# Performance work log

Hardware: AMD Instinct MI355X
Metric: run time of the kernel (lower is better)

Reference implementation:

```python
import jax, jax.numpy as jnp
import numpy as np

N_HEADS = 16


def setup_inputs() -> dict:
    key = jax.random.key(0)
    ks = jax.random.split(key, 10)
    B, M, N, C, D = 2, 2048, 2048, 1024, 1024
    s = 0.02
    return {
        "kv": jax.random.normal(ks[0], (B, M, C), jnp.float32),
        "q": jax.random.normal(ks[1], (B, N, D), jnp.float32),
        "Wk": jax.random.normal(ks[2], (C, D), jnp.float32) * s,
        "bk": jnp.zeros((D,), jnp.float32),
        "Wq": jax.random.normal(ks[3], (D, D), jnp.float32) * s,
        "bq": jnp.zeros((D,), jnp.float32),
        "Wv": jax.random.normal(ks[4], (C, D), jnp.float32) * s,
        "bv": jnp.zeros((D,), jnp.float32),
        "Wp": jax.random.normal(ks[5], (D, D), jnp.float32) * s,
        "bp": jnp.zeros((D,), jnp.float32),
    }


def reference(kv, q, Wk, bk, Wq, bq, Wv, bv, Wp, bp):
    B, M, C = kv.shape
    B2, N, D = q.shape
    H = N_HEADS
    hd = D // H
    # projections (weights stored as [in, out]; torch Linear is x @ W.T + b with W [out,in])
    k = (kv @ Wk + bk).reshape(B, M, H, hd).transpose(0, 2, 1, 3)  # [B,H,M,hd]
    qh = (q @ Wq + bq).reshape(B, N, H, hd).transpose(0, 2, 1, 3)  # [B,H,N,hd]
    v = (kv @ Wv + bv).reshape(B, M, H, hd).transpose(0, 2, 1, 3)  # [B,H,M,hd]
    scale = 1.0 / jnp.sqrt(jnp.asarray(hd, k.dtype))
    att = jnp.einsum("bhnd,bhmd->bhnm", qh, k) * scale
    att = jax.nn.softmax(att, axis=-1)
    y = jnp.einsum("bhnm,bhmd->bhnd", att, v)  # [B,H,N,hd]
    y = y.transpose(0, 2, 1, 3).reshape(B, N, D)
    return y @ Wp + bp
```

## Files before the change

kernel.cpp:

```cpp
#include <hip/hip_runtime.h>

#define DV 1024
#define HD 64

typedef short v4s __attribute__((ext_vector_type(4)));
typedef short v8s __attribute__((ext_vector_type(8)));
typedef float v4f __attribute__((ext_vector_type(4)));

__device__ __forceinline__ short f2bf(float x){
  unsigned u = __float_as_uint(x);
  u += 0x7FFFu + ((u >> 16) & 1u);
  return (short)(u >> 16);
}

__device__ __forceinline__ void async16(const void* g, void* l){
  __builtin_amdgcn_global_load_lds((const __attribute__((address_space(1))) void*)g,
                                   (__attribute__((address_space(3))) void*)l, 16, 0, 0);
}

__device__ __forceinline__ int swz(int lane){
  return (((lane & 7) ^ (lane >> 3)) << 3);
}

__global__ __launch_bounds__(256) void cvt2(const float* __restrict__ xa,
                                            const float* __restrict__ xb,
                                            short* __restrict__ ya,
                                            short* __restrict__ yb, int n){
  const float* x = blockIdx.y ? xb : xa;
  short* y = blockIdx.y ? yb : ya;
  int stride = gridDim.x * 256 * 4;
  for (int i = (blockIdx.x * 256 + threadIdx.x) * 4; i < n; i += stride){
    float4 v = *(const float4*)(x + i);
    v4s s; s.x = f2bf(v.x); s.y = f2bf(v.y); s.z = f2bf(v.z); s.w = f2bf(v.w);
    *(v4s*)(y + i) = s;
  }
}

__global__ __launch_bounds__(256) void tcvt4(
    const float* __restrict__ W0, const float* __restrict__ W1,
    const float* __restrict__ W2, const float* __restrict__ W3,
    short* __restrict__ T0, short* __restrict__ T1,
    short* __restrict__ T2, short* __restrict__ T3){
  const float* W; short* Wt;
  switch (blockIdx.z){
    case 0: W = W0; Wt = T0; break;
    case 1: W = W1; Wt = T1; break;
    case 2: W = W2; Wt = T2; break;
    default: W = W3; Wt = T3; break;
  }
  __shared__ short L[64 * 68];
  const int t = threadIdx.x;
  const int k0 = blockIdx.y * 64, n0 = blockIdx.x * 64;
  const int rr = t >> 4, cc = (t & 15) * 4;
  #pragma unroll
  for (int j = 0; j < 4; j++){
    int r = rr + j * 16;
    float4 v = *(const float4*)(W + (size_t)(k0 + r) * DV + n0 + cc);
    v4s s; s.x = f2bf(v.x); s.y = f2bf(v.y); s.z = f2bf(v.z); s.w = f2bf(v.w);
    *(v4s*)&L[r * 68 + cc] = s;
  }
  __syncthreads();
  #pragma unroll
  for (int j = 0; j < 4; j++){
    int n = rr + j * 16;
    v4s s;
    s.x = L[(cc + 0) * 68 + n];
    s.y = L[(cc + 1) * 68 + n];
    s.z = L[(cc + 2) * 68 + n];
    s.w = L[(cc + 3) * 68 + n];
    *(v4s*)(Wt + (size_t)(n0 + n) * DV + k0 + cc) = s;
  }
}

template<typename OUT_T>
__device__ __forceinline__ void gemm_tile(
    const short* __restrict__ A, const short* __restrict__ Bt,
    const float* __restrict__ bias, OUT_T* __restrict__ C,
    int M, int N, int K, float out_scale, int m0, int n0, bool bias_row)
{
  __shared__ short As[128 * 64];
  __shared__ short Bs[128 * 64];
  const int tid = threadIdx.x;
  const int wave = tid >> 6, lane = tid & 63;
  const int quad = lane >> 4, l15 = lane & 15;
  const int wr = (wave >> 1) * 64, wc = (wave & 1) * 64;
  const int srow = lane >> 3;
  const int sw = swz(lane);
  const v4f vzero = {0.f, 0.f, 0.f, 0.f};

  const short* pa[4]; const short* pb[4];
  #pragma unroll
  for (int ii = 0; ii < 4; ii++){
    int i = wave * 4 + ii;
    pa[ii] = A  + (size_t)(m0 + i * 8 + srow) * K + sw;
    pb[ii] = Bt + (size_t)(n0 + i * 8 + srow) * K + sw;
  }

  v8s ra[4], rb[4];
  #pragma unroll
  for (int ii = 0; ii < 4; ii++){
    ra[ii] = *(const v8s*)(pa[ii]);
    rb[ii] = *(const v8s*)(pb[ii]);
  }

  v4f acc[4][4];
  #pragma unroll
  for (int i = 0; i < 4; i++)
    #pragma unroll
    for (int j = 0; j < 4; j++)
      acc[i][j] = vzero;

  for (int kt = 0; kt < K; kt += 64){
    __syncthreads();
    #pragma unroll
    for (int ii = 0; ii < 4; ii++){
      int i = wave * 4 + ii;
      *(v8s*)&As[i * 512 + lane * 8] = ra[ii];
      *(v8s*)&Bs[i * 512 + lane * 8] = rb[ii];
    }
    __syncthreads();
    if (kt + 64 < K){
      #pragma unroll
      for (int ii = 0; ii < 4; ii++){
        ra[ii] = *(const v8s*)(pa[ii] + kt + 64);
        rb[ii] = *(const v8s*)(pb[ii] + kt + 64);
      }
    }
    #pragma unroll
    for (int ks = 0; ks < 2; ks++){
      v8s a[4], b[4];
      #pragma unroll
      for (int mt = 0; mt < 4; mt++)
        a[mt] = *(const v8s*)&As[(wr + mt * 16 + l15) * 64 + (((ks * 4 + quad) ^ (l15 & 7)) << 3)];
      #pragma unroll
      for (int nt = 0; nt < 4; nt++)
        b[nt] = *(const v8s*)&Bs[(wc + nt * 16 + l15) * 64 + (((ks * 4 + quad) ^ (l15 & 7)) << 3)];
      #pragma unroll
      for (int mt = 0; mt < 4; mt++)
        #pragma unroll
        for (int nt = 0; nt < 4; nt++)
          acc[mt][nt] = __builtin_amdgcn_mfma_f32_16x16x32_bf16(a[mt], b[nt], acc[mt][nt], 0, 0, 0);
    }
  }

  #pragma unroll
  for (int mt = 0; mt < 4; mt++){
    #pragma unroll
    for (int nt = 0; nt < 4; nt++){
      int row = m0 + wr + mt * 16 + quad * 4;
      int col = n0 + wc + nt * 16 + l15;
      float bcol = bias_row ? 0.0f : bias[col];
      #pragma unroll
      for (int r = 0; r < 4; r++){
        float bv = bias_row ? bias[row + r] : bcol;
        float v = (acc[mt][nt][r] + bv) * out_scale;
        if (sizeof(OUT_T) == 2)
          ((short*)C)[(size_t)(row + r) * N + col] = f2bf(v);
        else
          ((float*)C)[(size_t)(row + r) * N + col] = v;
      }
    }
  }
}

__global__ __launch_bounds__(256, 3) void proj3(
    const short* __restrict__ qb, const short* __restrict__ kvb,
    const short* __restrict__ Wqt, const short* __restrict__ Wkt,
    const short* __restrict__ Wvt,
    const float* __restrict__ bq, const float* __restrict__ bk,
    const float* __restrict__ bv,
    short* __restrict__ Qp, short* __restrict__ Kp, short* __restrict__ VT,
    float qscale)
{
  int bid = blockIdx.x;
  const short *A, *Bt; const float* bias; short* C;
  int M, N, m0, n0; float scale; bool brow;
  if (bid < 512){
    int z = bid >> 8, l = bid & 255;
    M = 4096; N = 1024; m0 = (l & 31) * 128; n0 = (l >> 5) * 128;
    A = z ? kvb : qb; Bt = z ? Wkt : Wqt; bias = z ? bk : bq;
    C = z ? Kp : Qp; scale = z ? 1.0f : qscale; brow = false;
  } else {
    int l = bid - 512;
    M = 1024; N = 4096; m0 = (l >> 5) * 128; n0 = (l & 31) * 128;
    A = Wvt; Bt = kvb; bias = bv; C = VT; scale = 1.0f; brow = true;
  }
  gemm_tile<short>(A, Bt, bias, C, M, N, 1024, scale, m0, n0, brow);
}

__global__ __launch_bounds__(256, 3) void gemm_f32(
    const short* __restrict__ A, const short* __restrict__ Bt,
    const float* __restrict__ bias, float* __restrict__ C)
{
  int bid = blockIdx.x;
  gemm_tile<float>(A, Bt, bias, C, 4096, 1024, 1024, 1.0f,
                   (bid & 31) * 128, (bid >> 5) * 128, false);
}

__global__ __launch_bounds__(256, 4) void attn(
    const short* __restrict__ Qp, const short* __restrict__ Kp,
    const short* __restrict__ Vt, short* __restrict__ Y)
{
  __shared__ short Qs[64 * 64];
  __shared__ short Ks[64 * 64];
  __shared__ short Vs[64 * 64];
  const int tid = threadIdx.x;
  const int wave = tid >> 6, lane = tid & 63;
  const int quad = lane >> 4, l15 = lane & 15;
  const int gid = blockIdx.x;
  const int qi = gid >> 5, bh = gid & 31;
  const int h = bh & 15, b = bh >> 4;
  const int n0 = qi * 64;
  const int srow = lane >> 3;
  const int sw = swz(lane);
  const size_t rowbase = (size_t)b * 2048;
  const v4f vzero = {0.f, 0.f, 0.f, 0.f};

  #pragma unroll
  for (int ii = 0; ii < 2; ii++){
    int i = wave * 2 + ii;
    async16(Qp + (rowbase + n0 + i * 8 + srow) * DV + h * HD + sw, &Qs[i * 512]);
  }

  const short* pk[2]; const short* pv[2];
  #pragma unroll
  for (int ii = 0; ii < 2; ii++){
    int i = wave * 2 + ii;
    pk[ii] = Kp + (rowbase + i * 8 + srow) * DV + h * HD + sw;
    pv[ii] = Vt + (size_t)(h * HD + i * 8 + srow) * 4096 + rowbase + sw;
  }
  v8s rk[2], rv[2];
  #pragma unroll
  for (int ii = 0; ii < 2; ii++){ rk[ii] = *(const v8s*)(pk[ii]); rv[ii] = *(const v8s*)(pv[ii]); }

  __syncthreads();

  v8s qf[2];
  #pragma unroll
  for (int ks = 0; ks < 2; ks++)
    qf[ks] = *(const v8s*)&Qs[(wave * 16 + l15) * 64 + (((ks * 4 + quad) ^ (l15 & 7)) << 3)];

  v4f o[4];
  #pragma unroll
  for (int dt = 0; dt < 4; dt++) o[dt] = vzero;
  float lsum = 0.0f;

  for (int kt = 0; kt < 32; kt++){
    __syncthreads();
    #pragma unroll
    for (int ii = 0; ii < 2; ii++){
      int i = wave * 2 + ii;
      *(v8s*)&Ks[i * 512 + lane * 8] = rk[ii];
      *(v8s*)&Vs[i * 512 + lane * 8] = rv[ii];
    }
    __syncthreads();
    if (kt < 31){
      #pragma unroll
      for (int ii = 0; ii < 2; ii++){
        rk[ii] = *(const v8s*)(pk[ii] + (size_t)(kt + 1) * 64 * DV);
        rv[ii] = *(const v8s*)(pv[ii] + (kt + 1) * 64);
      }
    }

    v4f s[4];
    #pragma unroll
    for (int kvt = 0; kvt < 4; kvt++) s[kvt] = vzero;
    #pragma unroll
    for (int ks = 0; ks < 2; ks++){
      v8s a[4];
      #pragma unroll
      for (int kvt = 0; kvt < 4; kvt++)
        a[kvt] = *(const v8s*)&Ks[(kvt * 16 + l15) * 64 + (((ks * 4 + quad) ^ (l15 & 7)) << 3)];
      #pragma unroll
      for (int kvt = 0; kvt < 4; kvt++)
        s[kvt] = __builtin_amdgcn_mfma_f32_16x16x32_bf16(a[kvt], qf[ks], s[kvt], 0, 0, 0);
    }

    v4s pf[4];
    #pragma unroll
    for (int kvt = 0; kvt < 4; kvt++){
      float p0 = __builtin_amdgcn_exp2f(s[kvt][0]);
      float p1 = __builtin_amdgcn_exp2f(s[kvt][1]);
      float p2 = __builtin_amdgcn_exp2f(s[kvt][2]);
      float p3 = __builtin_amdgcn_exp2f(s[kvt][3]);
      lsum += (p0 + p1) + (p2 + p3);
      v4s pk4; pk4.x = f2bf(p0); pk4.y = f2bf(p1); pk4.z = f2bf(p2); pk4.w = f2bf(p3);
      pf[kvt] = pk4;
    }

    #pragma unroll
    for (int ks = 0; ks < 4; ks++){
      v4s a[4];
      #pragma unroll
      for (int dt = 0; dt < 4; dt++){
        int vc = ks * 16 + quad * 4;
        a[dt] = *(const v4s*)&Vs[(dt * 16 + l15) * 64 + (((vc >> 3) ^ (l15 & 7)) << 3) + (vc & 7)];
      }
      #pragma unroll
      for (int dt = 0; dt < 4; dt++)
        o[dt] = __builtin_amdgcn_mfma_f32_16x16x16bf16_1k(a[dt], pf[ks], o[dt], 0, 0, 0);
    }
  }

  lsum += __shfl_xor(lsum, 16);
  lsum += __shfl_xor(lsum, 32);
  float inv = 1.0f / lsum;
  size_t row = rowbase + n0 + wave * 16 + l15;
  #pragma unroll
  for (int dt = 0; dt < 4; dt++){
    int col = h * HD + dt * 16 + quad * 4;
    unsigned p0 = (unsigned short)f2bf(o[dt][0] * inv) |
                  ((unsigned)(unsigned short)f2bf(o[dt][1] * inv) << 16);
    unsigned p1 = (unsigned short)f2bf(o[dt][2] * inv) |
                  ((unsigned)(unsigned short)f2bf(o[dt][3] * inv) << 16);
    *(unsigned*)(Y + row * DV + col)     = p0;
    *(unsigned*)(Y + row * DV + col + 2) = p1;
  }
}

extern "C" void kernel_launch(void* const* d_in, const int* in_sizes, int n_in,
                              void* d_out, int out_size, void* d_ws, size_t ws_size,
                              hipStream_t stream) {
  const float* kv = (const float*)d_in[0];
  const float* q  = (const float*)d_in[1];
  const float* Wk = (const float*)d_in[2];
  const float* bk = (const float*)d_in[3];
  const float* Wq = (const float*)d_in[4];
  const float* bq = (const float*)d_in[5];
  const float* Wv = (const float*)d_in[6];
  const float* bv = (const float*)d_in[7];
  const float* Wp = (const float*)d_in[8];
  const float* bp = (const float*)d_in[9];

  const size_t E  = 4194304;
  const size_t WE = 1048576;
  short* p   = (short*)d_ws;
  short* kvb = p; p += E;
  short* qb  = p; p += E;
  short* Wkt = p; p += WE;
  short* Wqt = p; p += WE;
  short* Wvt = p; p += WE;
  short* Wpt = p; p += WE;
  short* Kp  = p; p += E;
  short* Qp  = p; p += E;
  short* VT  = p; p += E;
  short* Yb  = p; p += E;

  cvt2<<<dim3(512, 2), 256, 0, stream>>>(kv, q, kvb, qb, (int)E);
  tcvt4<<<dim3(16, 16, 4), 256, 0, stream>>>(Wk, Wq, Wv, Wp, Wkt, Wqt, Wvt, Wpt);

  proj3<<<768, 256, 0, stream>>>(qb, kvb, Wqt, Wkt, Wvt, bq, bk, bv,
                                 Qp, Kp, VT, 0.18033688011f);

  attn<<<1024, 256, 0, stream>>>(Qp, Kp, VT, Yb);

  gemm_f32<<<256, 256, 0, stream>>>(Yb, Wpt, bp, (float*)d_out);
}
```

Before: 216.8 us.

## Rework attention tiling, bf16 packing and output GEMM tile shape

The attention kernel now processes two KV tiles per barrier pair with double-buffered register prefetch. It loads Q fragments directly from global memory instead of through LDS and stores V in padded rows rather than XOR swizzle. It also packs bf16 with a cheaper round-half-up and byte-permute, which slightly changes rounding. The output projection gets a dedicated 128x64-tile GEMM with twice as many blocks for better occupancy. These changes aim to reduce barrier count, instruction overhead and tail underutilization, at the cost of more registers and LDS.

```diff
diff --git a/kernel.cpp b/kernel.cpp
--- a/kernel.cpp
+++ b/kernel.cpp
@@ -6,16 +6,12 @@
 typedef short v4s __attribute__((ext_vector_type(4)));
 typedef short v8s __attribute__((ext_vector_type(8)));
 typedef float v4f __attribute__((ext_vector_type(4)));
+typedef int   v2i __attribute__((ext_vector_type(2)));
 
 __device__ __forceinline__ short f2bf(float x){
   unsigned u = __float_as_uint(x);
   u += 0x7FFFu + ((u >> 16) & 1u);
   return (short)(u >> 16);
-}
-
-__device__ __forceinline__ void async16(const void* g, void* l){
-  __builtin_amdgcn_global_load_lds((const __attribute__((address_space(1))) void*)g,
-                                   (__attribute__((address_space(3))) void*)l, 16, 0, 0);
 }
 
 __device__ __forceinline__ int swz(int lane){
@@ -188,22 +184,93 @@
   gemm_tile<short>(A, Bt, bias, C, M, N, 1024, scale, m0, n0, brow);
 }
 
-__global__ __launch_bounds__(256, 3) void gemm_f32(
+__global__ __launch_bounds__(256, 2) void gemm_f32(
     const short* __restrict__ A, const short* __restrict__ Bt,
     const float* __restrict__ bias, float* __restrict__ C)
 {
-  int bid = blockIdx.x;
-  gemm_tile<float>(A, Bt, bias, C, 4096, 1024, 1024, 1.0f,
-                   (bid & 31) * 128, (bid >> 5) * 128, false);
+  __shared__ short As[128 * 64];
+  __shared__ short Bs[64 * 64];
+  const int tid = threadIdx.x;
+  const int wave = tid >> 6, lane = tid & 63;
+  const int quad = lane >> 4, l15 = lane & 15;
+  const int bid = blockIdx.x;
+  const int m0 = (bid & 31) * 128, n0 = (bid >> 5) * 64;
+  const int wr = (wave >> 1) * 64, wc = (wave & 1) * 32;
+  const int srow = lane >> 3;
+  const int sw = swz(lane);
+  const int K = 1024;
+  const v4f vzero = {0.f, 0.f, 0.f, 0.f};
+
+  const short* pa[4]; const short* pb[2];
+  #pragma unroll
+  for (int ii = 0; ii < 4; ii++)
+    pa[ii] = A + (size_t)(m0 + (wave * 4 + ii) * 8 + srow) * K + sw;
+  #pragma unroll
+  for (int ii = 0; ii < 2; ii++)
+    pb[ii] = Bt + (size_t)(n0 + (wave * 2 + ii) * 8 + srow) * K + sw;
+
+  v8s ra[4], rb[2];
+  #pragma unroll
+  for (int ii = 0; ii < 4; ii++) ra[ii] = *(const v8s*)(pa[ii]);
+  #pragma unroll
+  for (int ii = 0; ii < 2; ii++) rb[ii] = *(const v8s*)(pb[ii]);
+
+  v4f acc[4][2];
+  #pragma unroll
+  for (int i = 0; i < 4; i++){ acc[i][0] = vzero; acc[i][1] = vzero; }
+
+  for (int kt = 0; kt < K; kt += 64){
+    __syncthreads();
+    #pragma unroll
+    for (int ii = 0; ii < 4; ii++)
+      *(v8s*)&As[(wave * 4 + ii) * 512 + lane * 8] = ra[ii];
+    #pragma unroll
+    for (int ii = 0; ii < 2; ii++)
+      *(v8s*)&Bs[(wave * 2 + ii) * 512 + lane * 8] = rb[ii];
+    __syncthreads();
+    if (kt + 64 < K){
+      #pragma unroll
+      for (int ii = 0; ii < 4; ii++) ra[ii] = *(const v8s*)(pa[ii] + kt + 64);
+      #pragma unroll
+      for (int ii = 0; ii < 2; ii++) rb[ii] = *(const v8s*)(pb[ii] + kt + 64);
+    }
+    #pragma unroll
+    for (int ks = 0; ks < 2; ks++){
+      v8s a[4], b[2];
+      #pragma unroll
+      for (int mt = 0; mt < 4; mt++)
+        a[mt] = *(const v8s*)&As[(wr + mt * 16 + l15) * 64 + (((ks * 4 + quad) ^ (l15 & 7)) << 3)];
+      #pragma unroll
+      for (int nt = 0; nt < 2; nt++)
+        b[nt] = *(const v8s*)&Bs[(wc + nt * 16 + l15) * 64 + (((ks * 4 + quad) ^ (l15 & 7)) << 3)];
+      #pragma unroll
+      for (int mt = 0; mt < 4; mt++)
+        #pragma unroll
+        for (int nt = 0; nt < 2; nt++)
+          acc[mt][nt] = __builtin_amdgcn_mfma_f32_16x16x32_bf16(a[mt], b[nt], acc[mt][nt], 0, 0, 0);
+    }
+  }
+
+  #pragma unroll
+  for (int mt = 0; mt < 4; mt++){
+    #pragma unroll
+    for (int nt = 0; nt < 2; nt++){
+      int row = m0 + wr + mt * 16 + quad * 4;
+      int col = n0 + wc + nt * 16 + l15;
+      float bcol = bias[col];
+      #pragma unroll
+      for (int r = 0; r < 4; r++)
+        C[(size_t)(row + r) * 1024 + col] = acc[mt][nt][r] + bcol;
+    }
+  }
 }
 
 __global__ __launch_bounds__(256, 4) void attn(
     const short* __restrict__ Qp, const short* __restrict__ Kp,
     const short* __restrict__ Vt, short* __restrict__ Y)
 {
-  __shared__ short Qs[64 * 64];
-  __shared__ short Ks[64 * 64];
-  __shared__ short Vs[64 * 64];
+  __shared__ short Ks[2][64 * 64];
+  __shared__ short Vs[2][64 * 72];
   const int tid = threadIdx.x;
   const int wave = tid >> 6, lane = tid & 63;
   const int quad = lane >> 4, l15 = lane & 15;
@@ -212,14 +279,16 @@
   const int h = bh & 15, b = bh >> 4;
   const int n0 = qi * 64;
   const int srow = lane >> 3;
+  const int c8 = (lane & 7) * 8;
   const int sw = swz(lane);
   const size_t rowbase = (size_t)b * 2048;
   const v4f vzero = {0.f, 0.f, 0.f, 0.f};
 
-  #pragma unroll
-  for (int ii = 0; ii < 2; ii++){
-    int i = wave * 2 + ii;
-    async16(Qp + (rowbase + n0 + i * 8 + srow) * DV + h * HD + sw, &Qs[i * 512]);
+  v8s qf[2];
+  {
+    const short* qrow = Qp + (rowbase + n0 + wave * 16 + l15) * DV + h * HD + quad * 8;
+    qf[0] = *(const v8s*)(qrow);
+    qf[1] = *(const v8s*)(qrow + 32);
   }
 
   const short* pk[2]; const short* pv[2];
@@ -227,78 +296,87 @@
   for (int ii = 0; ii < 2; ii++){
     int i = wave * 2 + ii;
     pk[ii] = Kp + (rowbase + i * 8 + srow) * DV + h * HD + sw;
-    pv[ii] = Vt + (size_t)(h * HD + i * 8 + srow) * 4096 + rowbase + sw;
-  }
-  v8s rk[2], rv[2];
-  #pragma unroll
-  for (int ii = 0; ii < 2; ii++){ rk[ii] = *(const v8s*)(pk[ii]); rv[ii] = *(const v8s*)(pv[ii]); }
-
-  __syncthreads();
-
-  v8s qf[2];
-  #pragma unroll
-  for (int ks = 0; ks < 2; ks++)
-    qf[ks] = *(const v8s*)&Qs[(wave * 16 + l15) * 64 + (((ks * 4 + quad) ^ (l15 & 7)) << 3)];
+    pv[ii] = Vt + (size_t)(h * HD + i * 8 + srow) * 4096 + rowbase + c8;
+  }
+  v8s rk[2][2], rv[2][2];
+  #pragma unroll
+  for (int tt = 0; tt < 2; tt++)
+    #pragma unroll
+    for (int ii = 0; ii < 2; ii++){
+      rk[tt][ii] = *(const v8s*)(pk[ii] + (size_t)tt * 64 * DV);
+      rv[tt][ii] = *(const v8s*)(pv[ii] + tt * 64);
+    }
 
   v4f o[4];
   #pragma unroll
   for (int dt = 0; dt < 4; dt++) o[dt] = vzero;
   float lsum = 0.0f;
 
-  for (int kt = 0; kt < 32; kt++){
-    __syncthreads();
-    #pragma unroll
-    for (int ii = 0; ii < 2; ii++){
-      int i = wave * 2 + ii;
-      *(v8s*)&Ks[i * 512 + lane * 8] = rk[ii];
-      *(v8s*)&Vs[i * 512 + lane * 8] = rv[ii];
-    }
-    __syncthreads();
-    if (kt < 31){
+  for (int t = 0; t < 16; t++){
+    __syncthreads();
+    #pragma unroll
+    for (int tt = 0; tt < 2; tt++)
       #pragma unroll
       for (int ii = 0; ii < 2; ii++){
-        rk[ii] = *(const v8s*)(pk[ii] + (size_t)(kt + 1) * 64 * DV);
-        rv[ii] = *(const v8s*)(pv[ii] + (kt + 1) * 64);
-      }
-    }
-
-    v4f s[4];
-    #pragma unroll
-    for (int kvt = 0; kvt < 4; kvt++) s[kvt] = vzero;
-    #pragma unroll
-    for (int ks = 0; ks < 2; ks++){
-      v8s a[4];
-      #pragma unroll
-      for (int kvt = 0; kvt < 4; kvt++)
-        a[kvt] = *(const v8s*)&Ks[(kvt * 16 + l15) * 64 + (((ks * 4 + quad) ^ (l15 & 7)) << 3)];
-      #pragma unroll
-      for (int kvt = 0; kvt < 4; kvt++)
-        s[kvt] = __builtin_amdgcn_mfma_f32_16x16x32_bf16(a[kvt], qf[ks], s[kvt], 0, 0, 0);
-    }
-
-    v4s pf[4];
-    #pragma unroll
-    for (int kvt = 0; kvt < 4; kvt++){
-      float p0 = __builtin_amdgcn_exp2f(s[kvt][0]);
-      float p1 = __builtin_amdgcn_exp2f(s[kvt][1]);
-      float p2 = __builtin_amdgcn_exp2f(s[kvt][2]);
-      float p3 = __builtin_amdgcn_exp2f(s[kvt][3]);
-      lsum += (p0 + p1) + (p2 + p3);
-      v4s pk4; pk4.x = f2bf(p0); pk4.y = f2bf(p1); pk4.z = f2bf(p2); pk4.w = f2bf(p3);
-      pf[kvt] = pk4;
-    }
-
-    #pragma unroll
-    for (int ks = 0; ks < 4; ks++){
-      v4s a[4];
-      #pragma unroll
-      for (int dt = 0; dt < 4; dt++){
-        int vc = ks * 16 + quad * 4;
-        a[dt] = *(const v4s*)&Vs[(dt * 16 + l15) * 64 + (((vc >> 3) ^ (l15 & 7)) << 3) + (vc & 7)];
-      }
-      #pragma unroll
-      for (int dt = 0; dt < 4; dt++)
-        o[dt] = __builtin_amdgcn_mfma_f32_16x16x16bf16_1k(a[dt], pf[ks], o[dt], 0, 0, 0);
+        int i = wave * 2 + ii;
+        *(v8s*)&Ks[tt][i * 512 + lane * 8] = rk[tt][ii];
+        *(v8s*)&Vs[tt][(i * 8 + srow) * 72 + c8] = rv[tt][ii];
+      }
+    __syncthreads();
+    if (t < 15){
+      #pragma unroll
+      for (int tt = 0; tt < 2; tt++)
+        #pragma unroll
+        for (int ii = 0; ii < 2; ii++){
+          rk[tt][ii] = *(const v8s*)(pk[ii] + (size_t)(2 * t + 2 + tt) * 64 * DV);
+          rv[tt][ii] = *(const v8s*)(pv[ii] + (2 * t + 2 + tt) * 64);
+        }
+    }
+
+    #pragma unroll
+    for (int tt = 0; tt < 2; tt++){
+      v4f s[4];
+      #pragma unroll
+      for (int kvt = 0; kvt < 4; kvt++) s[kvt] = vzero;
+      #pragma unroll
+      for (int ks = 0; ks < 2; ks++){
+        v8s a[4];
+        #pragma unroll
+        for (int kvt = 0; kvt < 4; kvt++)
+          a[kvt] = *(const v8s*)&Ks[tt][(kvt * 16 + l15) * 64 + (((ks * 4 + quad) ^ (l15 & 7)) << 3)];
+        #pragma unroll
+        for (int kvt = 0; kvt < 4; kvt++)
+          s[kvt] = __builtin_amdgcn_mfma_f32_16x16x32_bf16(a[kvt], qf[ks], s[kvt], 0, 0, 0);
+      }
+
+      v4s pf[4];
+      #pragma unroll
+      for (int kvt = 0; kvt < 4; kvt++){
+        float p0 = __builtin_amdgcn_exp2f(s[kvt][0]);
+        float p1 = __builtin_amdgcn_exp2f(s[kvt][1]);
+        float p2 = __builtin_amdgcn_exp2f(s[kvt][2]);
+        float p3 = __builtin_amdgcn_exp2f(s[kvt][3]);
+        lsum += (p0 + p1) + (p2 + p3);
+        unsigned u0 = __float_as_uint(p0) + 0x8000u;
+        unsigned u1 = __float_as_uint(p1) + 0x8000u;
+        unsigned u2 = __float_as_uint(p2) + 0x8000u;
+        unsigned u3 = __float_as_uint(p3) + 0x8000u;
+        v2i pi;
+        pi.x = (int)__builtin_amdgcn_perm(u1, u0, 0x07060302u);
+        pi.y = (int)__builtin_amdgcn_perm(u3, u2, 0x07060302u);
+        pf[kvt] = __builtin_bit_cast(v4s, pi);
+      }
+
+      #pragma unroll
+      for (int ks = 0; ks < 4; ks++){
+        v4s a[4];
+        #pragma unroll
+        for (int dt = 0; dt < 4; dt++)
+          a[dt] = *(const v4s*)&Vs[tt][(dt * 16 + l15) * 72 + ks * 16 + quad * 4];
+        #pragma unroll
+        for (int dt = 0; dt < 4; dt++)
+          o[dt] = __builtin_amdgcn_mfma_f32_16x16x16bf16_1k(a[dt], pf[ks], o[dt], 0, 0, 0);
+      }
     }
   }
 
@@ -354,5 +432,5 @@
 
   attn<<<1024, 256, 0, stream>>>(Qp, Kp, VT, Yb);
 
-  gemm_f32<<<256, 256, 0, stream>>>(Yb, Wpt, bp, (float*)d_out);
-}
+  gemm_f32<<<512, 256, 0, stream>>>(Yb, Wpt, bp, (float*)d_out);
+}
```

After: 232.2 us. 7.1% more time.
